# Performance work log

Hardware: AMD Instinct MI355X
Metric: run time of the kernel (lower is better)

## Reference

```python
import jax, jax.numpy as jnp
import numpy as np

COMMITMENT_COST = 0.25


def setup_inputs() -> dict:
    key = jax.random.key(0)
    k1, k2 = jax.random.split(key)
    B, S, D, K = 8, 4096, 256, 1024
    inputs = jax.random.normal(k1, (B, S, D), dtype=jnp.float32)
    attention_mask = jnp.ones((B, S), dtype=jnp.float32)
    codebook = jax.random.normal(k2, (K, D), dtype=jnp.float32)
    return {"inputs": inputs, "attention_mask": attention_mask, "codebook": codebook}


def reference(inputs, attention_mask, codebook):
    # Inference-mode forward of VectorQuantizer (no EMA update / init / revival).
    B, S, D = inputs.shape
    z = inputs.astype(jnp.float32).reshape(-1, D)          # (N, D)
    m = attention_mask.reshape(-1).astype(jnp.float32)     # (N,)

    cb = codebook.astype(jnp.float32)                      # (K, D)
    # squared L2 distances: ||z||^2 - 2 z e^T + ||e||^2
    dist = (jnp.sum(z * z, axis=-1, keepdims=True)
            - 2.0 * jnp.matmul(z, cb.T)
            + jnp.sum(cb * cb, axis=-1)[None, :])          # (N, K)
    idx = jnp.argmin(dist, axis=-1)                        # (N,)
    q = cb[idx]                                            # (N, D) codebook lookup

    n_valid = jnp.sum(m)
    # mse over valid tokens (elementwise mean, matching F.mse_loss on flat_valid)
    diff = z - jax.lax.stop_gradient(q)
    commitment = jnp.sum(m[:, None] * diff * diff) / (n_valid * D)
    vq_loss = COMMITMENT_COST * commitment

    # straight-through estimator; invalid positions zeroed (as in torch scatter)
    q_ste = z + jax.lax.stop_gradient(q - z)
    quantized = (q_ste * m[:, None]).reshape(B, S, D)
    indices = jnp.where(m > 0, idx, 0).reshape(B, S)
    return quantized, vq_loss, indices
```

## Files before the change

### kernel.cpp

```cpp
#include <hip/hip_runtime.h>
#include <cstdint>

typedef short bf16x8 __attribute__((ext_vector_type(8)));
typedef float f32x4  __attribute__((ext_vector_type(4)));

#define TOK    64
#define CH     64
#define NCH    16
#define BUFW   16384
#define MAXC   32

__device__ __forceinline__ unsigned short f2bf(float f) {
  unsigned u = __float_as_uint(f);
  return (unsigned short)((u + 0x7FFFu + ((u >> 16) & 1u)) >> 16);
}
__device__ __forceinline__ uint4 pack8(float4 a, float4 b) {
  uint4 u;
  u.x = (unsigned)f2bf(a.x) | ((unsigned)f2bf(a.y) << 16);
  u.y = (unsigned)f2bf(a.z) | ((unsigned)f2bf(a.w) << 16);
  u.z = (unsigned)f2bf(b.x) | ((unsigned)f2bf(b.y) << 16);
  u.w = (unsigned)f2bf(b.z) | ((unsigned)f2bf(b.w) << 16);
  return u;
}
__device__ __forceinline__ void gload16(const unsigned short* g, unsigned short* l) {
  __builtin_amdgcn_global_load_lds(
      (const __attribute__((address_space(1))) unsigned int*)(const void*)g,
      (__attribute__((address_space(3))) unsigned int*)(void*)l, 16, 0, 0);
}

__global__ __launch_bounds__(256) void vq_prep(const float* __restrict__ cb,
                                               unsigned short* __restrict__ cb_bf,
                                               float* __restrict__ ee,
                                               float* __restrict__ acc2,
                                               int* __restrict__ done_ctr, int K) {
  if (blockIdx.x == 0 && threadIdx.x == 0) {
    acc2[0] = 0.f; acc2[1] = 0.f; *done_ctr = 0;
  }
  int wave = threadIdx.x >> 6, lane = threadIdx.x & 63;
  int k = blockIdx.x * 4 + wave;
  if (k >= K) return;
  float4 v = *reinterpret_cast<const float4*>(cb + (size_t)k * 256 + lane * 4);
  float s = v.x * v.x + v.y * v.y + v.z * v.z + v.w * v.w;
  #pragma unroll
  for (int off = 32; off; off >>= 1) s += __shfl_down(s, off, 64);
  ushort4 b;
  b.x = f2bf(v.x); b.y = f2bf(v.y); b.z = f2bf(v.z); b.w = f2bf(v.w);
  *reinterpret_cast<ushort4*>(cb_bf + (size_t)k * 256 + lane * 4) = b;
  if (lane == 0) ee[k] = s;
}

__global__ __launch_bounds__(256, 2) void vq_main(
    const float* __restrict__ z, const float* __restrict__ cb,
    const unsigned short* __restrict__ cb_bf, const float* __restrict__ ee,
    const float* __restrict__ mask,
    float* __restrict__ out_q, float* __restrict__ out_idx_f,
    float* __restrict__ out_loss, float* __restrict__ acc2,
    int* __restrict__ done_ctr, int nblocks, int K) {
  __shared__ __align__(16) unsigned short sbuf[2 * BUFW];
  __shared__ float ee_lds[1024];
  __shared__ float znorm[TOK];
  __shared__ int   ccnt[TOK];
  __shared__ unsigned umin[TOK];
  __shared__ unsigned cand[TOK * MAXC];
  __shared__ unsigned short bkbuf[TOK];
  __shared__ float red[8];
  __shared__ bool  last;

  const int t = threadIdx.x;
  const int n0 = blockIdx.x * TOK;
  const int wv = t >> 6, lane = t & 63;
  const int quad = lane >> 4, l15 = lane & 15;
  const int q16 = t & 15;

  float ea = ee[t], eb = ee[t + 256], ec = ee[t + 512], ed = ee[t + 768];
  ee_lds[t] = ea; ee_lds[t + 256] = eb; ee_lds[t + 512] = ec; ee_lds[t + 768] = ed;
  if (t < TOK) { ccnt[t] = 0; umin[t] = 0x7F7FFFFFu; }
  float em = fmaxf(fmaxf(ea, eb), fmaxf(ec, ed));
  #pragma unroll
  for (int off = 32; off; off >>= 1) em = fmaxf(em, __shfl_xor(em, off, 64));
  if (lane == 0) red[wv] = em;

  #pragma unroll
  for (int pass = 0; pass < 4; ++pass) {
    int row = pass * 16 + (t >> 4);
    const float* zr = z + (size_t)(n0 + row) * 256;
    float ssq = 0.f;
    #pragma unroll
    for (int j = 0; j < 2; ++j) {
      float4 a = *reinterpret_cast<const float4*>(zr + q16 * 16 + j * 8);
      float4 b = *reinterpret_cast<const float4*>(zr + q16 * 16 + j * 8 + 4);
      ssq += a.x*a.x + a.y*a.y + a.z*a.z + a.w*a.w
           + b.x*b.x + b.y*b.y + b.z*b.z + b.w*b.w;
      int g = q16 * 2 + j;
      *reinterpret_cast<uint4*>(&sbuf[row * 256 + ((g ^ (row & 7)) * 8)]) = pack8(a, b);
    }
    #pragma unroll
    for (int off = 1; off < 16; off <<= 1) ssq += __shfl_xor(ssq, off, 64);
    if (q16 == 0) znorm[row] = sqrtf(ssq);
  }
  __syncthreads();

  const float enmax = sqrtf(fmaxf(fmaxf(red[0], red[1]), fmaxf(red[2], red[3])));

  bf16x8 afrag[8];
  float  znreg[4];
  {
    int row = wv * 16 + l15;
    #pragma unroll
    for (int kk = 0; kk < 8; ++kk) {
      int g = (quad + kk * 4) ^ (row & 7);
      afrag[kk] = *reinterpret_cast<const bf16x8*>(&sbuf[row * 256 + g * 8]);
    }
    #pragma unroll
    for (int r = 0; r < 4; ++r)
      znreg[r] = znorm[wv * 16 + quad * 4 + r];
  }
  __syncthreads();

  {
    #pragma unroll
    for (int i = 0; i < 8; ++i) {
      int f = (wv * 8 + i) * 64 + lane;
      int row = f >> 5, slot = f & 31;
      gload16(cb_bf + (size_t)row * 256 + ((slot ^ (row & 7)) * 8),
              &sbuf[(size_t)(wv * 512 + i * 64) * 8]);
    }
  }
  asm volatile("s_waitcnt vmcnt(0)" ::: "memory");
  __syncthreads();

  for (int lc = 0; lc < NCH; ++lc) {
    const int kbase = lc * CH;
    unsigned short* cur = &sbuf[(lc & 1) * BUFW];
    unsigned short* nxt = &sbuf[((lc + 1) & 1) * BUFW];
    if (lc < NCH - 1) {
      const unsigned short* base = cb_bf + (size_t)(kbase + CH) * 256;
      #pragma unroll
      for (int i = 0; i < 8; ++i) {
        int f = (wv * 8 + i) * 64 + lane;
        int row = f >> 5, slot = f & 31;
        gload16(base + (size_t)row * 256 + ((slot ^ (row & 7)) * 8),
                nxt + (size_t)(wv * 512 + i * 64) * 8);
      }
    }

    f32x4 acc[4];
    #pragma unroll
    for (int ct = 0; ct < 4; ++ct) acc[ct] = (f32x4){0.f, 0.f, 0.f, 0.f};
    __builtin_amdgcn_s_setprio(1);
    #pragma unroll
    for (int kk = 0; kk < 8; ++kk) {
      int gx = quad + kk * 4;
      bf16x8 b0 = *reinterpret_cast<const bf16x8*>(&cur[(l15)      * 256 + ((gx ^ ( l15       & 7)) * 8)]);
      bf16x8 b1 = *reinterpret_cast<const bf16x8*>(&cur[(16 + l15) * 256 + ((gx ^ ((16 + l15) & 7)) * 8)]);
      bf16x8 b2 = *reinterpret_cast<const bf16x8*>(&cur[(32 + l15) * 256 + ((gx ^ ((32 + l15) & 7)) * 8)]);
      bf16x8 b3 = *reinterpret_cast<const bf16x8*>(&cur[(48 + l15) * 256 + ((gx ^ ((48 + l15) & 7)) * 8)]);
      acc[0] = __builtin_amdgcn_mfma_f32_16x16x32_bf16(afrag[kk], b0, acc[0], 0, 0, 0);
      acc[1] = __builtin_amdgcn_mfma_f32_16x16x32_bf16(afrag[kk], b1, acc[1], 0, 0, 0);
      acc[2] = __builtin_amdgcn_mfma_f32_16x16x32_bf16(afrag[kk], b2, acc[2], 0, 0, 0);
      acc[3] = __builtin_amdgcn_mfma_f32_16x16x32_bf16(afrag[kk], b3, acc[3], 0, 0, 0);
    }
    __builtin_amdgcn_s_setprio(0);

    float e0 = ee_lds[kbase + l15],      e1 = ee_lds[kbase + 16 + l15];
    float e2 = ee_lds[kbase + 32 + l15], e3 = ee_lds[kbase + 48 + l15];
    float en0 = sqrtf(e0), en1 = sqrtf(e1), en2 = sqrtf(e2), en3 = sqrtf(e3);
    #pragma unroll
    for (int r = 0; r < 4; ++r) {
      float d0 = e0 - 2.f * acc[0][r];
      float d1 = e1 - 2.f * acc[1][r];
      float d2 = e2 - 2.f * acc[2][r];
      float d3 = e3 - 2.f * acc[3][r];
      int tok = wv * 16 + quad * 4 + r;
      float dm = fmaxf(fminf(fminf(d0, d1), fminf(d2, d3)), 0.f);
      atomicMin(&umin[tok], __float_as_uint(dm));
      float am = __uint_as_float(umin[tok]);
      float zn = znreg[r];
      if (d0 <= am + 1.5f + 0.002f * zn * en0) {
        int sl = atomicAdd(&ccnt[tok], 1);
        if (sl < MAXC) cand[tok * MAXC + sl] =
            (__float_as_uint(fmaxf(d0, 0.f)) & 0xFFFFFC00u) | (unsigned)(kbase + l15);
      }
      if (d1 <= am + 1.5f + 0.002f * zn * en1) {
        int sl = atomicAdd(&ccnt[tok], 1);
        if (sl < MAXC) cand[tok * MAXC + sl] =
            (__float_as_uint(fmaxf(d1, 0.f)) & 0xFFFFFC00u) | (unsigned)(kbase + 16 + l15);
      }
      if (d2 <= am + 1.5f + 0.002f * zn * en2) {
        int sl = atomicAdd(&ccnt[tok], 1);
        if (sl < MAXC) cand[tok * MAXC + sl] =
            (__float_as_uint(fmaxf(d2, 0.f)) & 0xFFFFFC00u) | (unsigned)(kbase + 32 + l15);
      }
      if (d3 <= am + 1.5f + 0.002f * zn * en3) {
        int sl = atomicAdd(&ccnt[tok], 1);
        if (sl < MAXC) cand[tok * MAXC + sl] =
            (__float_as_uint(fmaxf(d3, 0.f)) & 0xFFFFFC00u) | (unsigned)(kbase + 48 + l15);
      }
    }
    asm volatile("s_waitcnt vmcnt(0)" ::: "memory");
    __syncthreads();
  }

  for (int it = 0; it < 16; ++it) {
    int tok = wv * 16 + it;
    int n = n0 + tok;
    int cnt = ccnt[tok];
    int bk = 0;
    if (cnt > MAXC) {
      float4 zv = *reinterpret_cast<const float4*>(z + (size_t)n * 256 + lane * 4);
      float bs = 3.4e38f;
      for (int k = 0; k < K; k += 2) {
        float4 ca = *reinterpret_cast<const float4*>(cb + (size_t)k * 256 + lane * 4);
        float4 cbv = *reinterpret_cast<const float4*>(cb + (size_t)(k + 1) * 256 + lane * 4);
        float pa = zv.x * ca.x + zv.y * ca.y + zv.z * ca.z + zv.w * ca.w;
        float pb = zv.x * cbv.x + zv.y * cbv.y + zv.z * cbv.z + zv.w * cbv.w;
        #pragma unroll
        for (int off = 32; off; off >>= 1) {
          pa += __shfl_xor(pa, off, 64);
          pb += __shfl_xor(pb, off, 64);
        }
        float sa = ee_lds[k] - 2.f * pa;
        float sb = ee_lds[k + 1] - 2.f * pb;
        if (sa < bs) { bs = sa; bk = k; }
        if (sb < bs) { bs = sb; bk = k + 1; }
      }
    } else {
      float thr = __uint_as_float(umin[tok]) + 1.5f + 0.002f * znorm[tok] * enmax;
      int c = (lane < cnt) ? lane : 0;
      unsigned pe = cand[tok * MAXC + c];
      bool flag = (lane < cnt) && (__uint_as_float(pe & 0xFFFFFC00u) <= thr);
      unsigned long long msk = __ballot(flag);
      if (__popcll(msk) == 1) {
        int cc = __ffsll((long long)msk) - 1;
        bk = (int)(cand[tok * MAXC + cc] & 1023u);
      } else {
        float4 zv = *reinterpret_cast<const float4*>(z + (size_t)n * 256 + lane * 4);
        float bs = 3.4e38f; bk = 1 << 29;
        int cc = 0;
        for (; cc + 4 <= cnt; cc += 4) {
          int k0 = cand[tok * MAXC + cc]     & 1023;
          int k1 = cand[tok * MAXC + cc + 1] & 1023;
          int k2 = cand[tok * MAXC + cc + 2] & 1023;
          int k3 = cand[tok * MAXC + cc + 3] & 1023;
          float4 e0 = *reinterpret_cast<const float4*>(cb + (size_t)k0 * 256 + lane * 4);
          float4 e1 = *reinterpret_cast<const float4*>(cb + (size_t)k1 * 256 + lane * 4);
          float4 e2 = *reinterpret_cast<const float4*>(cb + (size_t)k2 * 256 + lane * 4);
          float4 e3 = *reinterpret_cast<const float4*>(cb + (size_t)k3 * 256 + lane * 4);
          float p0 = zv.x * e0.x + zv.y * e0.y + zv.z * e0.z + zv.w * e0.w;
          float p1 = zv.x * e1.x + zv.y * e1.y + zv.z * e1.z + zv.w * e1.w;
          float p2 = zv.x * e2.x + zv.y * e2.y + zv.z * e2.z + zv.w * e2.w;
          float p3 = zv.x * e3.x + zv.y * e3.y + zv.z * e3.z + zv.w * e3.w;
          #pragma unroll
          for (int off = 32; off; off >>= 1) {
            p0 += __shfl_xor(p0, off, 64);
            p1 += __shfl_xor(p1, off, 64);
            p2 += __shfl_xor(p2, off, 64);
            p3 += __shfl_xor(p3, off, 64);
          }
          float s0 = ee_lds[k0] - 2.f * p0;
          float s1 = ee_lds[k1] - 2.f * p1;
          float s2 = ee_lds[k2] - 2.f * p2;
          float s3 = ee_lds[k3] - 2.f * p3;
          if (s0 < bs || (s0 == bs && k0 < bk)) { bs = s0; bk = k0; }
          if (s1 < bs || (s1 == bs && k1 < bk)) { bs = s1; bk = k1; }
          if (s2 < bs || (s2 == bs && k2 < bk)) { bs = s2; bk = k2; }
          if (s3 < bs || (s3 == bs && k3 < bk)) { bs = s3; bk = k3; }
        }
        for (; cc < cnt; ++cc) {
          int k = cand[tok * MAXC + cc] & 1023;
          float4 ev = *reinterpret_cast<const float4*>(cb + (size_t)k * 256 + lane * 4);
          float dp = zv.x * ev.x + zv.y * ev.y + zv.z * ev.z + zv.w * ev.w;
          #pragma unroll
          for (int off = 32; off; off >>= 1) dp += __shfl_xor(dp, off, 64);
          float s = ee_lds[k] - 2.f * dp;
          if (s < bs || (s == bs && k < bk)) { bs = s; bk = k; }
        }
      }
    }
    bkbuf[tok] = (unsigned short)bk;
  }

  float lsum = 0.f, msum = 0.f;
  for (int it = 0; it < 16; it += 2) {
    int tokA = wv * 16 + it, tokB = tokA + 1;
    int na = n0 + tokA, nb = n0 + tokB;
    int ba = bkbuf[tokA], bb = bkbuf[tokB];
    float4 za = *reinterpret_cast<const float4*>(z + (size_t)na * 256 + lane * 4);
    float4 zb = *reinterpret_cast<const float4*>(z + (size_t)nb * 256 + lane * 4);
    float4 qa = *reinterpret_cast<const float4*>(cb + (size_t)ba * 256 + lane * 4);
    float4 qb = *reinterpret_cast<const float4*>(cb + (size_t)bb * 256 + lane * 4);
    float ma = mask[na], mb = mask[nb];
    float4 oa; oa.x = qa.x * ma; oa.y = qa.y * ma; oa.z = qa.z * ma; oa.w = qa.w * ma;
    float4 ob; ob.x = qb.x * mb; ob.y = qb.y * mb; ob.z = qb.z * mb; ob.w = qb.w * mb;
    *reinterpret_cast<float4*>(out_q + (size_t)na * 256 + lane * 4) = oa;
    *reinterpret_cast<float4*>(out_q + (size_t)nb * 256 + lane * 4) = ob;
    float dxa = za.x - qa.x, dya = za.y - qa.y, dza = za.z - qa.z, dwa = za.w - qa.w;
    float dxb = zb.x - qb.x, dyb = zb.y - qb.y, dzb = zb.z - qb.z, dwb = zb.w - qb.w;
    lsum = fmaf(ma, dxa * dxa + dya * dya + dza * dza + dwa * dwa, lsum);
    lsum = fmaf(mb, dxb * dxb + dyb * dyb + dzb * dzb + dwb * dwb, lsum);
    if (lane == 0) {
      msum += ma + mb;
      out_idx_f[na] = (ma > 0.f) ? (float)ba : 0.f;
      out_idx_f[nb] = (mb > 0.f) ? (float)bb : 0.f;
    }
  }
  #pragma unroll
  for (int off = 32; off; off >>= 1) lsum += __shfl_down(lsum, off, 64);
  if (lane == 0) { red[wv] = lsum; red[4 + wv] = msum; }
  __syncthreads();
  if (t == 0) {
    atomicAdd(&acc2[0], red[0] + red[1] + red[2] + red[3]);
    atomicAdd(&acc2[1], red[4] + red[5] + red[6] + red[7]);
    __threadfence();
    int prev = atomicAdd(done_ctr, 1);
    last = (prev == nblocks - 1);
  }
  __syncthreads();
  if (last && t == 0) {
    float s  = atomicAdd(&acc2[0], 0.0f);
    float nv = atomicAdd(&acc2[1], 0.0f);
    out_loss[0] = (nv > 0.f) ? (0.25f * s / (nv * 256.0f)) : 0.0f;
  }
}

extern "C" void kernel_launch(void* const* d_in, const int* in_sizes, int n_in,
                              void* d_out, int out_size, void* d_ws, size_t ws_size,
                              hipStream_t stream) {
  const float* z    = (const float*)d_in[0];
  const float* mask = (const float*)d_in[1];
  const float* cb   = (const float*)d_in[2];
  const int N = in_sizes[1];
  const int D = 256;
  const int K = in_sizes[2] / D;

  float* wsf  = (float*)d_ws;
  float* acc2 = wsf;
  int*   dctr = (int*)(wsf + 2);
  float* ee   = wsf + 8;
  unsigned short* cb_bf = (unsigned short*)(ee + K);

  float* out_q     = (float*)d_out;
  float* out_loss  = out_q + (size_t)N * D;
  float* out_idx_f = out_loss + 1;

  vq_prep<<<(K + 3) / 4, 256, 0, stream>>>(cb, cb_bf, ee, acc2, dctr, K);
  vq_main<<<N / TOK, 256, 0, stream>>>(z, cb, cb_bf, ee, mask, out_q,
                                       out_idx_f, out_loss, acc2, dctr, N / TOK, K);
}
```

Baseline: 165.0 us.

## Switch distance GEMM to 32x32x16 MFMA with per-lane token candidate filtering

Replaces the four 16x16x32 MFMAs per k-step with one 32x32x16 MFMA. Each wave now covers 32 tokens by 32 codes, and the token operand is held in registers while codebook rows are read from LDS. Because each lane owns one token, candidate selection computes a per-lane minimum and does one atomicMin per chunk instead of one per row. A coarse check against the largest codebook norm skips the per-code candidate tests in most chunks. The aim is fewer LDS reads and fewer shared atomics per chunk, at the cost of higher register pressure from the 16-fragment token tile and the 16-wide accumulator.

```diff
diff --git a/kernel.cpp b/kernel.cpp
--- a/kernel.cpp
+++ b/kernel.cpp
@@ -2,7 +2,7 @@
 #include <cstdint>
 
 typedef short bf16x8 __attribute__((ext_vector_type(8)));
-typedef float f32x4  __attribute__((ext_vector_type(4)));
+typedef float f32x16 __attribute__((ext_vector_type(16)));
 
 #define TOK    64
 #define CH     64
@@ -69,7 +69,8 @@
   const int t = threadIdx.x;
   const int n0 = blockIdx.x * TOK;
   const int wv = t >> 6, lane = t & 63;
-  const int quad = lane >> 4, l15 = lane & 15;
+  const int ts = wv & 1, cs = wv >> 1;
+  const int l31 = lane & 31, hk = lane >> 5;
   const int q16 = t & 15;
 
   float ea = ee[t], eb = ee[t + 256], ec = ee[t + 512], ed = ee[t + 768];
@@ -102,19 +103,16 @@
 
   const float enmax = sqrtf(fmaxf(fmaxf(red[0], red[1]), fmaxf(red[2], red[3])));
 
-  bf16x8 afrag[8];
-  float  znreg[4];
+  bf16x8 tfrag[16];
   {
-    int row = wv * 16 + l15;
-    #pragma unroll
-    for (int kk = 0; kk < 8; ++kk) {
-      int g = (quad + kk * 4) ^ (row & 7);
-      afrag[kk] = *reinterpret_cast<const bf16x8*>(&sbuf[row * 256 + g * 8]);
-    }
-    #pragma unroll
-    for (int r = 0; r < 4; ++r)
-      znreg[r] = znorm[wv * 16 + quad * 4 + r];
-  }
+    int row = ts * 32 + l31;
+    #pragma unroll
+    for (int kk = 0; kk < 16; ++kk) {
+      int g = (kk * 2 + hk) ^ (row & 7);
+      tfrag[kk] = *reinterpret_cast<const bf16x8*>(&sbuf[row * 256 + g * 8]);
+    }
+  }
+  const float zn = znorm[ts * 32 + l31];
   __syncthreads();
 
   {
@@ -128,6 +126,9 @@
   }
   asm volatile("s_waitcnt vmcnt(0)" ::: "memory");
   __syncthreads();
+
+  float am = 3.4e38f;
+  const int tok = ts * 32 + l31;
 
   for (int lc = 0; lc < NCH; ++lc) {
     const int kbase = lc * CH;
@@ -144,57 +145,52 @@
       }
     }
 
-    f32x4 acc[4];
-    #pragma unroll
-    for (int ct = 0; ct < 4; ++ct) acc[ct] = (f32x4){0.f, 0.f, 0.f, 0.f};
+    f32x16 acc = (f32x16){0.f};
+    const int arow = cs * 32 + l31;
+    const unsigned short* abase = &cur[arow * 256];
+    const int asw = arow & 7;
     __builtin_amdgcn_s_setprio(1);
     #pragma unroll
-    for (int kk = 0; kk < 8; ++kk) {
-      int gx = quad + kk * 4;
-      bf16x8 b0 = *reinterpret_cast<const bf16x8*>(&cur[(l15)      * 256 + ((gx ^ ( l15       & 7)) * 8)]);
-      bf16x8 b1 = *reinterpret_cast<const bf16x8*>(&cur[(16 + l15) * 256 + ((gx ^ ((16 + l15) & 7)) * 8)]);
-      bf16x8 b2 = *reinterpret_cast<const bf16x8*>(&cur[(32 + l15) * 256 + ((gx ^ ((32 + l15) & 7)) * 8)]);
-      bf16x8 b3 = *reinterpret_cast<const bf16x8*>(&cur[(48 + l15) * 256 + ((gx ^ ((48 + l15) & 7)) * 8)]);
-      acc[0] = __builtin_amdgcn_mfma_f32_16x16x32_bf16(afrag[kk], b0, acc[0], 0, 0, 0);
-      acc[1] = __builtin_amdgcn_mfma_f32_16x16x32_bf16(afrag[kk], b1, acc[1], 0, 0, 0);
-      acc[2] = __builtin_amdgcn_mfma_f32_16x16x32_bf16(afrag[kk], b2, acc[2], 0, 0, 0);
-      acc[3] = __builtin_amdgcn_mfma_f32_16x16x32_bf16(afrag[kk], b3, acc[3], 0, 0, 0);
+    for (int kk = 0; kk < 16; ++kk) {
+      bf16x8 a = *reinterpret_cast<const bf16x8*>(abase + (((kk * 2 + hk) ^ asw) * 8));
+      acc = __builtin_amdgcn_mfma_f32_32x32x16_bf16(a, tfrag[kk], acc, 0, 0, 0);
     }
     __builtin_amdgcn_s_setprio(0);
 
-    float e0 = ee_lds[kbase + l15],      e1 = ee_lds[kbase + 16 + l15];
-    float e2 = ee_lds[kbase + 32 + l15], e3 = ee_lds[kbase + 48 + l15];
-    float en0 = sqrtf(e0), en1 = sqrtf(e1), en2 = sqrtf(e2), en3 = sqrtf(e3);
-    #pragma unroll
-    for (int r = 0; r < 4; ++r) {
-      float d0 = e0 - 2.f * acc[0][r];
-      float d1 = e1 - 2.f * acc[1][r];
-      float d2 = e2 - 2.f * acc[2][r];
-      float d3 = e3 - 2.f * acc[3][r];
-      int tok = wv * 16 + quad * 4 + r;
-      float dm = fmaxf(fminf(fminf(d0, d1), fminf(d2, d3)), 0.f);
-      atomicMin(&umin[tok], __float_as_uint(dm));
-      float am = __uint_as_float(umin[tok]);
-      float zn = znreg[r];
-      if (d0 <= am + 1.5f + 0.002f * zn * en0) {
-        int sl = atomicAdd(&ccnt[tok], 1);
-        if (sl < MAXC) cand[tok * MAXC + sl] =
-            (__float_as_uint(fmaxf(d0, 0.f)) & 0xFFFFFC00u) | (unsigned)(kbase + l15);
-      }
-      if (d1 <= am + 1.5f + 0.002f * zn * en1) {
-        int sl = atomicAdd(&ccnt[tok], 1);
-        if (sl < MAXC) cand[tok * MAXC + sl] =
-            (__float_as_uint(fmaxf(d1, 0.f)) & 0xFFFFFC00u) | (unsigned)(kbase + 16 + l15);
-      }
-      if (d2 <= am + 1.5f + 0.002f * zn * en2) {
-        int sl = atomicAdd(&ccnt[tok], 1);
-        if (sl < MAXC) cand[tok * MAXC + sl] =
-            (__float_as_uint(fmaxf(d2, 0.f)) & 0xFFFFFC00u) | (unsigned)(kbase + 32 + l15);
-      }
-      if (d3 <= am + 1.5f + 0.002f * zn * en3) {
-        int sl = atomicAdd(&ccnt[tok], 1);
-        if (sl < MAXC) cand[tok * MAXC + sl] =
-            (__float_as_uint(fmaxf(d3, 0.f)) & 0xFFFFFC00u) | (unsigned)(kbase + 48 + l15);
+    const int cb0 = kbase + cs * 32 + hk * 4;
+    float4 ee4[4];
+    #pragma unroll
+    for (int gg = 0; gg < 4; ++gg)
+      ee4[gg] = *reinterpret_cast<const float4*>(&ee_lds[cb0 + 8 * gg]);
+
+    float dm = 3.4e38f;
+    #pragma unroll
+    for (int gg = 0; gg < 4; ++gg) {
+      float d0 = ee4[gg].x - 2.f * acc[gg * 4 + 0];
+      float d1 = ee4[gg].y - 2.f * acc[gg * 4 + 1];
+      float d2 = ee4[gg].z - 2.f * acc[gg * 4 + 2];
+      float d3 = ee4[gg].w - 2.f * acc[gg * 4 + 3];
+      dm = fminf(dm, fminf(fminf(d0, d1), fminf(d2, d3)));
+    }
+    dm = fmaxf(dm, 0.f);
+    atomicMin(&umin[tok], __float_as_uint(dm));
+    am = fminf(am, __uint_as_float(umin[tok]));
+
+    if (dm <= am + 1.5f + 0.002f * zn * enmax) {
+      #pragma unroll
+      for (int gg = 0; gg < 4; ++gg) {
+        #pragma unroll
+        for (int jj = 0; jj < 4; ++jj) {
+          float eej = (jj == 0) ? ee4[gg].x : (jj == 1) ? ee4[gg].y
+                    : (jj == 2) ? ee4[gg].z : ee4[gg].w;
+          float d = eej - 2.f * acc[gg * 4 + jj];
+          if (d <= am + 1.5f + 0.002f * zn * sqrtf(eej)) {
+            int code = cb0 + 8 * gg + jj;
+            int sl = atomicAdd(&ccnt[tok], 1);
+            if (sl < MAXC) cand[tok * MAXC + sl] =
+                (__float_as_uint(fmaxf(d, 0.f)) & 0xFFFFFC00u) | (unsigned)code;
+          }
+        }
       }
     }
     asm volatile("s_waitcnt vmcnt(0)" ::: "memory");
@@ -202,9 +198,9 @@
   }
 
   for (int it = 0; it < 16; ++it) {
-    int tok = wv * 16 + it;
-    int n = n0 + tok;
-    int cnt = ccnt[tok];
+    int tk = wv * 16 + it;
+    int n = n0 + tk;
+    int cnt = ccnt[tk];
     int bk = 0;
     if (cnt > MAXC) {
       float4 zv = *reinterpret_cast<const float4*>(z + (size_t)n * 256 + lane * 4);
@@ -225,23 +221,23 @@
         if (sb < bs) { bs = sb; bk = k + 1; }
       }
     } else {
-      float thr = __uint_as_float(umin[tok]) + 1.5f + 0.002f * znorm[tok] * enmax;
+      float thr = __uint_as_float(umin[tk]) + 1.5f + 0.002f * znorm[tk] * enmax;
       int c = (lane < cnt) ? lane : 0;
-      unsigned pe = cand[tok * MAXC + c];
+      unsigned pe = cand[tk * MAXC + c];
       bool flag = (lane < cnt) && (__uint_as_float(pe & 0xFFFFFC00u) <= thr);
       unsigned long long msk = __ballot(flag);
       if (__popcll(msk) == 1) {
         int cc = __ffsll((long long)msk) - 1;
-        bk = (int)(cand[tok * MAXC + cc] & 1023u);
+        bk = (int)(cand[tk * MAXC + cc] & 1023u);
       } else {
         float4 zv = *reinterpret_cast<const float4*>(z + (size_t)n * 256 + lane * 4);
         float bs = 3.4e38f; bk = 1 << 29;
         int cc = 0;
         for (; cc + 4 <= cnt; cc += 4) {
-          int k0 = cand[tok * MAXC + cc]     & 1023;
-          int k1 = cand[tok * MAXC + cc + 1] & 1023;
-          int k2 = cand[tok * MAXC + cc + 2] & 1023;
-          int k3 = cand[tok * MAXC + cc + 3] & 1023;
+          int k0 = cand[tk * MAXC + cc]     & 1023;
+          int k1 = cand[tk * MAXC + cc + 1] & 1023;
+          int k2 = cand[tk * MAXC + cc + 2] & 1023;
+          int k3 = cand[tk * MAXC + cc + 3] & 1023;
           float4 e0 = *reinterpret_cast<const float4*>(cb + (size_t)k0 * 256 + lane * 4);
           float4 e1 = *reinterpret_cast<const float4*>(cb + (size_t)k1 * 256 + lane * 4);
           float4 e2 = *reinterpret_cast<const float4*>(cb + (size_t)k2 * 256 + lane * 4);
@@ -267,7 +263,7 @@
           if (s3 < bs || (s3 == bs && k3 < bk)) { bs = s3; bk = k3; }
         }
         for (; cc < cnt; ++cc) {
-          int k = cand[tok * MAXC + cc] & 1023;
+          int k = cand[tk * MAXC + cc] & 1023;
           float4 ev = *reinterpret_cast<const float4*>(cb + (size_t)k * 256 + lane * 4);
           float dp = zv.x * ev.x + zv.y * ev.y + zv.z * ev.z + zv.w * ev.w;
           #pragma unroll
@@ -277,7 +273,7 @@
         }
       }
     }
-    bkbuf[tok] = (unsigned short)bk;
+    bkbuf[tk] = (unsigned short)bk;
   }
 
   float lsum = 0.f, msum = 0.f;
```

Result: no change. 162.2 us (-1.7%).
